# Kernel optimization log

Measured on AMD Instinct MI355X. Metric: run time of the kernel, lower is better.

The kernel has to match this reference:

```python
import jax, jax.numpy as jnp
import numpy as np

N_EMBD = 2048
N_HEAD = 16
N_INNER = 8192
EPS = 1e-5


def _wn_weight(v, g):
    # torch weight_norm with dim=1 on weight [out, in]:
    # w[:, j] = g[j] * v[:, j] / ||v[:, j]||_2
    norm = jnp.sqrt(jnp.sum(v * v, axis=0))  # [in]
    return v * (g / norm)[None, :]


def _layer_norm(x, gamma, beta):
    mu = jnp.mean(x, axis=-1, keepdims=True)
    var = jnp.mean(jnp.square(x - mu), axis=-1, keepdims=True)
    return (x - mu) * jax.lax.rsqrt(var + EPS) * gamma + beta


def setup_inputs() -> dict:
    key = jax.random.key(0)
    ks = jax.random.split(key, 12)
    E, I, H = N_EMBD, N_INNER, N_HEAD
    s = lambda n: 1.0 / np.sqrt(n)
    return {
        "hidden_states": jax.random.normal(ks[0], (2, 2048, E), jnp.float32),
        "ln1_g": jnp.ones((E,), jnp.float32),
        "ln1_b": jnp.zeros((E,), jnp.float32),
        "w_qkv": jax.random.normal(ks[1], (3 * E, E), jnp.float32) * s(E),
        "b_qkv": jnp.zeros((3 * E,), jnp.float32),
        "attn_proj_v": jax.random.normal(ks[2], (E, E), jnp.float32) * s(E),
        "attn_proj_g": jnp.abs(jax.random.normal(ks[3], (E,), jnp.float32)) + 0.5,
        "attn_proj_b": jnp.zeros((E,), jnp.float32),
        "emotion_bias": jax.random.normal(ks[4], (H,), jnp.float32) * 0.1,
        "ln2_g": jnp.ones((E,), jnp.float32),
        "ln2_b": jnp.zeros((E,), jnp.float32),
        "w_fc": jax.random.normal(ks[5], (I, E), jnp.float32) * s(E),
        "b_fc": jnp.zeros((I,), jnp.float32),
        "mlp_proj_v": jax.random.normal(ks[6], (E, I), jnp.float32) * s(I),
        "mlp_proj_g": jnp.abs(jax.random.normal(ks[7], (I,), jnp.float32)) + 0.5,
        "mlp_proj_b": jnp.zeros((E,), jnp.float32),
    }


def reference(hidden_states, ln1_g, ln1_b, w_qkv, b_qkv, attn_proj_v, attn_proj_g,
              attn_proj_b, emotion_bias, ln2_g, ln2_b, w_fc, b_fc,
              mlp_proj_v, mlp_proj_g, mlp_proj_b):
    B, S, E = hidden_states.shape
    H = N_HEAD
    D = E // H

    # --- attention sub-block ---
    residual = hidden_states
    x = _layer_norm(hidden_states, ln1_g, ln1_b)
    qkv = x @ w_qkv.T + b_qkv                       # [B,S,3E]
    q, k, v = jnp.split(qkv, 3, axis=-1)
    q = q.reshape(B, S, H, D).transpose(0, 2, 1, 3)  # [B,H,S,D]
    k = k.reshape(B, S, H, D).transpose(0, 2, 1, 3)
    v = v.reshape(B, S, H, D).transpose(0, 2, 1, 3)

    scores = jnp.einsum("bhqd,bhkd->bhqk", q, k) / jnp.sqrt(jnp.float32(D))
    scores = scores + emotion_bias[None, :, None, None]
    probs = jax.nn.softmax(scores, axis=-1)
    attn = jnp.einsum("bhqk,bhkd->bhqd", probs, v)   # [B,H,S,D]
    attn = attn.transpose(0, 2, 1, 3).reshape(B, S, E)
    w_proj = _wn_weight(attn_proj_v, attn_proj_g)
    attn = attn @ w_proj.T + attn_proj_b

    hidden = attn + residual

    # --- MLP sub-block ---
    residual = hidden
    x = _layer_norm(hidden, ln2_g, ln2_b)
    h = jax.nn.gelu(x @ w_fc.T + b_fc, approximate=False)
    w_proj2 = _wn_weight(mlp_proj_v, mlp_proj_g)
    h = h @ w_proj2.T + mlp_proj_b
    return residual + h
```

## Files before the change

### kernel.cpp

```cpp
#include <hip/hip_runtime.h>
#include <hip/hip_bf16.h>

#define DEVI __device__ __forceinline__

typedef __attribute__((ext_vector_type(8))) __bf16 bf16x8;
typedef __attribute__((ext_vector_type(4))) float f32x4;
typedef __attribute__((ext_vector_type(4))) unsigned short u16x4;
typedef __attribute__((ext_vector_type(8))) unsigned short u16x8;

DEVI unsigned short f2bf(float f) {
  unsigned int u = __float_as_uint(f);
  u += 0x7FFFu + ((u >> 16) & 1u);
  return (unsigned short)(u >> 16);
}
DEVI float bf2f(unsigned short u) {
  return __uint_as_float(((unsigned int)u) << 16);
}

#define GLD16(g, l) __builtin_amdgcn_global_load_lds(                      \
    (const __attribute__((address_space(1))) void*)(g),                    \
    (__attribute__((address_space(3))) void*)(l), 16, 0, 0)


__global__ __launch_bounds__(256) void cast_k(const float* __restrict__ in,
                                              unsigned short* __restrict__ out,
                                              int n4) {
  for (int i = blockIdx.x * 256 + threadIdx.x; i < n4; i += gridDim.x * 256) {
    f32x4 v = ((const f32x4*)in)[i];
    u16x4 o;
    o.x = f2bf(v.x); o.y = f2bf(v.y); o.z = f2bf(v.z); o.w = f2bf(v.w);
    ((u16x4*)out)[i] = o;
  }
}

__global__ __launch_bounds__(256) void colnorm1_k(const float* __restrict__ v,
                                                  float* __restrict__ part,
                                                  int cols) {
  const int tid = threadIdx.x;
  const int g = tid & 127;
  const int s = tid >> 7;
  const int c0 = blockIdx.x * 512;
  const int r0 = blockIdx.y * 64 + s * 32;
  const float* base = v + (size_t)r0 * cols + c0 + g * 4;
  f32x4 acc = {};
#pragma unroll 4
  for (int i = 0; i < 32; ++i) {
    f32x4 x = *(const f32x4*)(base + (size_t)i * cols);
    acc.x += x.x * x.x; acc.y += x.y * x.y;
    acc.z += x.z * x.z; acc.w += x.w * x.w;
  }
  __shared__ f32x4 red[256];
  red[tid] = acc;
  __syncthreads();
  if (s == 0) {
    f32x4 a = red[tid], b = red[tid + 128];
    f32x4 o;
    o.x = a.x + b.x; o.y = a.y + b.y; o.z = a.z + b.z; o.w = a.w + b.w;
    *(f32x4*)(part + (size_t)blockIdx.y * cols + c0 + g * 4) = o;
  }
}

__global__ __launch_bounds__(256) void colnorm2_k(const float* __restrict__ part,
                                                  const float* __restrict__ g,
                                                  float* __restrict__ s,
                                                  int cols, int nrc) {
  const int c = blockIdx.x * 256 + threadIdx.x;
  float acc = 0.f;
  for (int i = 0; i < nrc; ++i) acc += part[(size_t)i * cols + c];
  s[c] = g[c] * rsqrtf(acc);
}

__global__ __launch_bounds__(256) void scale_cast_k(const float* __restrict__ in,
                                                    const float* __restrict__ s,
                                                    unsigned short* __restrict__ out,
                                                    int cols, int n4) {
  const int cmask4 = (cols >> 2) - 1;
  for (int i = blockIdx.x * 256 + threadIdx.x; i < n4; i += gridDim.x * 256) {
    f32x4 v = ((const f32x4*)in)[i];
    f32x4 sv = ((const f32x4*)s)[i & cmask4];
    u16x4 o;
    o.x = f2bf(v.x * sv.x); o.y = f2bf(v.y * sv.y);
    o.z = f2bf(v.z * sv.z); o.w = f2bf(v.w * sv.w);
    ((u16x4*)out)[i] = o;
  }
}

__global__ __launch_bounds__(256) void ln_k(const float* __restrict__ x,
                                            const float* __restrict__ g,
                                            const float* __restrict__ b,
                                            unsigned short* __restrict__ out) {
  const int tid = threadIdx.x, lane = tid & 63, wid = tid >> 6;
  const int row = blockIdx.x;
  const float* xr = x + (size_t)row * 2048;
  f32x4 a0 = ((const f32x4*)xr)[tid];
  f32x4 a1 = ((const f32x4*)xr)[tid + 256];
  float s = a0.x + a0.y + a0.z + a0.w + a1.x + a1.y + a1.z + a1.w;
  float ss = a0.x * a0.x + a0.y * a0.y + a0.z * a0.z + a0.w * a0.w +
             a1.x * a1.x + a1.y * a1.y + a1.z * a1.z + a1.w * a1.w;
#pragma unroll
  for (int m = 1; m < 64; m <<= 1) {
    s += __shfl_xor(s, m);
    ss += __shfl_xor(ss, m);
  }
  __shared__ float red[8];
  if (lane == 0) { red[wid] = s; red[4 + wid] = ss; }
  __syncthreads();
  s = red[0] + red[1] + red[2] + red[3];
  ss = red[4] + red[5] + red[6] + red[7];
  const float mu = s * (1.f / 2048.f);
  const float var = ss * (1.f / 2048.f) - mu * mu;
  const float rs = rsqrtf(var + 1e-5f);
  f32x4 g0 = ((const f32x4*)g)[tid], g1 = ((const f32x4*)g)[tid + 256];
  f32x4 b0 = ((const f32x4*)b)[tid], b1 = ((const f32x4*)b)[tid + 256];
  u16x4 o0, o1;
  o0.x = f2bf((a0.x - mu) * rs * g0.x + b0.x);
  o0.y = f2bf((a0.y - mu) * rs * g0.y + b0.y);
  o0.z = f2bf((a0.z - mu) * rs * g0.z + b0.z);
  o0.w = f2bf((a0.w - mu) * rs * g0.w + b0.w);
  o1.x = f2bf((a1.x - mu) * rs * g1.x + b1.x);
  o1.y = f2bf((a1.y - mu) * rs * g1.y + b1.y);
  o1.z = f2bf((a1.z - mu) * rs * g1.z + b1.z);
  o1.w = f2bf((a1.w - mu) * rs * g1.w + b1.w);
  unsigned short* orow = out + (size_t)row * 2048;
  *(u16x4*)(orow + 4 * tid) = o0;
  *(u16x4*)(orow + 1024 + 4 * tid) = o1;
}

__global__ __launch_bounds__(256) void vtrans_k(const unsigned short* __restrict__ qkv,
                                                unsigned short* __restrict__ vt) {
  __shared__ unsigned short t[64][134];
  const int tid = threadIdx.x;
  const int bh = blockIdx.x >> 5, st = blockIdx.x & 31;
  const int b = bh >> 4, h = bh & 15;
  const unsigned short* vb = qkv + (size_t)(b * 2048 + st * 64) * 6144 + 4096 + h * 128;
#pragma unroll
  for (int i = 0; i < 4; ++i) {
    int f = tid + (i << 8);
    int row = f >> 4, c8 = f & 15;
    u16x8 x = *(const u16x8*)(vb + (size_t)row * 6144 + c8 * 8);
#pragma unroll
    for (int j = 0; j < 4; ++j) {
      unsigned int pk = ((unsigned int)x[2 * j + 1] << 16) | x[2 * j];
      *(unsigned int*)&t[row][c8 * 8 + 2 * j] = pk;
    }
  }
  __syncthreads();
  const int lane = tid & 63, wid = tid >> 6;
  unsigned short* ob = vt + ((size_t)bh << 18) + (st << 6);
#pragma unroll
  for (int j = 0; j < 32; ++j) {
    int d = (wid << 5) + j;
    ob[((size_t)d << 11) + lane] = t[lane][d];
  }
}

__global__ __launch_bounds__(256) void g4red_k(const unsigned short* __restrict__ parts,
                                               const float* __restrict__ bias,
                                               const float* __restrict__ res,
                                               float* __restrict__ out, int n4) {
  const size_t PS = (size_t)4096 * 2048;
  for (int i = blockIdx.x * 256 + threadIdx.x; i < n4; i += gridDim.x * 256) {
    u16x4 a = ((const u16x4*)(parts))[i];
    u16x4 b = ((const u16x4*)(parts + PS))[i];
    u16x4 c = ((const u16x4*)(parts + 2 * PS))[i];
    u16x4 d = ((const u16x4*)(parts + 3 * PS))[i];
    f32x4 r = ((const f32x4*)res)[i];
    f32x4 bb = ((const f32x4*)bias)[i & 511];
    f32x4 o;
    o.x = bf2f(a.x) + bf2f(b.x) + bf2f(c.x) + bf2f(d.x) + r.x + bb.x;
    o.y = bf2f(a.y) + bf2f(b.y) + bf2f(c.y) + bf2f(d.y) + r.y + bb.y;
    o.z = bf2f(a.z) + bf2f(b.z) + bf2f(c.z) + bf2f(d.z) + r.z + bb.z;
    o.w = bf2f(a.w) + bf2f(b.w) + bf2f(c.w) + bf2f(d.w) + r.w + bb.w;
    ((f32x4*)out)[i] = o;
  }
}

struct GemmP {
  const unsigned short* A;
  const unsigned short* B;
  const float* bias;
  const float* res;
  float* outF;
  unsigned short* outH;
  int M, N, K;
};

DEVI void gemm128_body(const GemmP& p, int m0, int n0, int k0, int nk) {
  const int tid = threadIdx.x, lane = tid & 63, wid = tid >> 6;
  const int K = p.K;
  const int wr = wid >> 1, wc = wid & 1;

  __shared__ __align__(16) unsigned short sA[2][4096];
  __shared__ __align__(16) unsigned short sB[2][4096];

  const int c0 = tid, c1 = tid + 256;
  const unsigned short* gA0 = p.A + (size_t)(m0 + (c0 >> 2)) * K + k0 + ((c0 & 3) << 3);
  const unsigned short* gA1 = p.A + (size_t)(m0 + (c1 >> 2)) * K + k0 + ((c1 & 3) << 3);
  const unsigned short* gB0 = p.B + (size_t)(n0 + (c0 >> 2)) * K + k0 + ((c0 & 3) << 3);
  const unsigned short* gB1 = p.B + (size_t)(n0 + (c1 >> 2)) * K + k0 + ((c1 & 3) << 3);
  const int l0 = wid << 9, l1 = (wid << 9) + 2048;

  f32x4 acc[4][4] = {};
  const int arow = (wr << 6) + (lane & 15);
  const int brow = (wc << 6) + (lane & 15);
  const int koff = (lane >> 4) << 3;

#define STAGE128(bufi, t) do { int ko = (t) << 5;       \
    GLD16(gA0 + ko, &sA[bufi][l0]);                     \
    GLD16(gA1 + ko, &sA[bufi][l1]);                     \
    GLD16(gB0 + ko, &sB[bufi][l0]);                     \
    GLD16(gB1 + ko, &sB[bufi][l1]); } while (0)

  STAGE128(0, 0);
  __syncthreads();
  int cur = 0;
  for (int t = 0; t < nk; ++t) {
    if (t + 1 < nk) STAGE128(cur ^ 1, t + 1);
    bf16x8 af[4], bfr[4];
#pragma unroll
    for (int i = 0; i < 4; ++i)
      af[i] = *(const bf16x8*)&sA[cur][(arow + (i << 4)) * 32 + koff];
#pragma unroll
    for (int i = 0; i < 4; ++i)
      bfr[i] = *(const bf16x8*)&sB[cur][(brow + (i << 4)) * 32 + koff];
#pragma unroll
    for (int i = 0; i < 4; ++i)
#pragma unroll
      for (int j = 0; j < 4; ++j)
        acc[i][j] = __builtin_amdgcn_mfma_f32_16x16x32_bf16(af[i], bfr[j], acc[i][j], 0, 0, 0);
    __syncthreads();
    cur ^= 1;
  }
#undef STAGE128

  const int rbase = m0 + (wr << 6) + ((lane >> 4) << 2);
  const int cbase = n0 + (wc << 6) + (lane & 15);
#pragma unroll
  for (int mi = 0; mi < 4; ++mi) {
#pragma unroll
    for (int ni = 0; ni < 4; ++ni) {
      const int col = cbase + (ni << 4);
#pragma unroll
      for (int r = 0; r < 4; ++r) {
        const int row = rbase + (mi << 4) + r;
        const size_t o = (size_t)row * p.N + col;
        p.outF[o] = acc[mi][ni][r] + p.bias[col] + p.res[o];
      }
    }
  }
}

__global__ __launch_bounds__(256) void g2_proj128(GemmP p) {
  const int x = blockIdx.x & 7, i = blockIdx.x >> 3;
  const int bm = (x >> 1) * 8 + (i >> 3);
  const int bn = (x & 1) * 8 + (i & 7);
  gemm128_body(p, bm << 7, bn << 7, 0, p.K >> 5);
}

DEVI void setup256(const GemmP& p, int m0, int n0, int k0,
                   const unsigned short*& gsA0, const unsigned short*& gsA1,
                   const unsigned short*& gsB0, const unsigned short*& gsB1) {
  const int tid = threadIdx.x;
  int r_[2], c_[2];
#pragma unroll
  for (int j = 0; j < 2; ++j) {
    int d = tid * 16 + j * 8192;
    int w = (d & 1023) ^ (((d >> 9) & 1) << 5);
    r_[j] = ((d >> 10) << 4) + (w >> 6);
    c_[j] = (w & 63) >> 1;
  }
  gsA0 = p.A + (size_t)(m0 + r_[0]) * p.K + k0 + c_[0];
  gsA1 = p.A + (size_t)(m0 + r_[1]) * p.K + k0 + c_[1];
  gsB0 = p.B + (size_t)(n0 + r_[0]) * p.K + k0 + c_[0];
  gsB1 = p.B + (size_t)(n0 + r_[1]) * p.K + k0 + c_[1];
}

template <int EPI>
DEVI void epi256(const GemmP& p, f32x4 (&acc)[8][4], int m0, int n0,
                 unsigned short* outH) {
  const int lane = threadIdx.x & 63, wid = threadIdx.x >> 6;
  const int wr = wid >> 2, wc = wid & 3;
  const int lr = lane & 15, lk = lane >> 4;
  const int rbase = m0 + wr * 128 + (lk << 2);
  const int cbase = n0 + wc * 64 + lr;
#pragma unroll
  for (int m = 0; m < 8; ++m) {
#pragma unroll
    for (int n = 0; n < 4; ++n) {
      const int col = cbase + (n << 4);
      const float bb = (EPI == 5) ? 0.f : p.bias[col];
#pragma unroll
      for (int r = 0; r < 4; ++r) {
        const int row = rbase + (m << 4) + r;
        float v = acc[m][n][r] + bb;
        if constexpr (EPI == 2) {
          float y = 0.7978845608028654f * (v + 0.044715f * v * v * v);
          float u = __expf(2.f * y);
          v = (y > 40.f) ? v : v * (u / (u + 1.f));
        }
        outH[(size_t)row * p.N + col] = f2bf(v);
      }
    }
  }
}

DEVI void gemm8p_body(const GemmP& p, unsigned short* lds_raw, int m0, int n0) {
  const int tid = threadIdx.x, lane = tid & 63, wid = tid >> 6;
  const int wr = wid >> 2, wc = wid & 3;
  const int lr = lane & 15, lk = lane >> 4;
  const int fb = (lr * 64 + lk * 16) ^ ((lr & 8) << 2);

  const unsigned short *gsA0, *gsA1, *gsB0, *gsB1;
  setup256(p, m0, n0, 0, gsA0, gsA1, gsB0, gsB1);

#define STAGE_A8(b, kt) do { unsigned short* _d = lds_raw + ((b) << 14);       \
    GLD16(gsA0 + ((size_t)(kt) << 5), _d + (tid << 3));                        \
    GLD16(gsA1 + ((size_t)(kt) << 5), _d + 4096 + (tid << 3)); } while (0)
#define STAGE_B8(b, kt) do { unsigned short* _d = lds_raw + ((b) << 14) + 8192;\
    GLD16(gsB0 + ((size_t)(kt) << 5), _d + (tid << 3));                        \
    GLD16(gsB1 + ((size_t)(kt) << 5), _d + 4096 + (tid << 3)); } while (0)

  f32x4 acc[8][4] = {};
  const int NK = p.K >> 5;

  STAGE_A8(0, 0); STAGE_B8(0, 0);
  STAGE_A8(1, 1); STAGE_B8(1, 1);
  STAGE_A8(2, 2); STAGE_B8(2, 2);
  asm volatile("s_waitcnt vmcnt(8)" ::: "memory");
  __builtin_amdgcn_s_barrier();

  for (int t = 0; t < NK; ++t) {
    const int bi = t & 3;
    const char* tA = (const char*)(lds_raw + (bi << 14));
    const char* tB = (const char*)(lds_raw + (bi << 14) + 8192);
    bf16x8 a_[4], b_[4];
#pragma unroll
    for (int n = 0; n < 4; ++n)
      b_[n] = *(const bf16x8*)(tB + (((wc << 2) + n) << 10) + fb);
#pragma unroll
    for (int m = 0; m < 4; ++m)
      a_[m] = *(const bf16x8*)(tA + (((wr << 3) + m) << 10) + fb);
    if (t + 3 < NK) STAGE_A8((t + 3) & 3, t + 3);
    __builtin_amdgcn_s_barrier();
    asm volatile("s_waitcnt lgkmcnt(0)" ::: "memory");
    __builtin_amdgcn_sched_barrier(0);
    __builtin_amdgcn_s_setprio(1);
#pragma unroll
    for (int m = 0; m < 4; ++m)
#pragma unroll
      for (int n = 0; n < 4; ++n)
        acc[m][n] = __builtin_amdgcn_mfma_f32_16x16x32_bf16(a_[m], b_[n], acc[m][n], 0, 0, 0);
    __builtin_amdgcn_s_setprio(0);
    __builtin_amdgcn_s_barrier();
#pragma unroll
    for (int m = 0; m < 4; ++m)
      a_[m] = *(const bf16x8*)(tA + (((wr << 3) + 4 + m) << 10) + fb);
    if (t + 3 < NK) STAGE_B8((t + 3) & 3, t + 3);
    if (t + 3 < NK)      asm volatile("s_waitcnt vmcnt(8)" ::: "memory");
    else if (t + 2 < NK) asm volatile("s_waitcnt vmcnt(4)" ::: "memory");
    else if (t + 1 < NK) asm volatile("s_waitcnt vmcnt(0)" ::: "memory");
    __builtin_amdgcn_s_barrier();
    asm volatile("s_waitcnt lgkmcnt(0)" ::: "memory");
    __builtin_amdgcn_sched_barrier(0);
    __builtin_amdgcn_s_setprio(1);
#pragma unroll
    for (int m = 0; m < 4; ++m)
#pragma unroll
      for (int n = 0; n < 4; ++n)
        acc[4 + m][n] = __builtin_amdgcn_mfma_f32_16x16x32_bf16(a_[m], b_[n], acc[4 + m][n], 0, 0, 0);
    __builtin_amdgcn_s_setprio(0);
    __builtin_amdgcn_s_barrier();
  }
#undef STAGE_A8
#undef STAGE_B8
  epi256<2>(p, acc, m0, n0, p.outH);
}

template <int EPI>
DEVI void gemm2p_body(const GemmP& p, unsigned short* lds_raw, int m0, int n0,
                      int k0, int nk, unsigned short* outH) {
  const int tid = threadIdx.x, lane = tid & 63, wid = tid >> 6;
  const int wr = wid >> 2, wc = wid & 3;
  const int lr = lane & 15, lk = lane >> 4;
  const int fb = (lr * 64 + lk * 16) ^ ((lr & 8) << 2);

  const unsigned short *gsA0, *gsA1, *gsB0, *gsB1;
  setup256(p, m0, n0, k0, gsA0, gsA1, gsB0, gsB1);

#define STG2(b, kt) do { unsigned short* _d = lds_raw + ((b) << 14);     \
    GLD16(gsA0 + ((size_t)(kt) << 5), _d + (tid << 3));                  \
    GLD16(gsA1 + ((size_t)(kt) << 5), _d + 4096 + (tid << 3));           \
    GLD16(gsB0 + ((size_t)(kt) << 5), _d + 8192 + (tid << 3));           \
    GLD16(gsB1 + ((size_t)(kt) << 5), _d + 12288 + (tid << 3)); } while (0)

  f32x4 acc[8][4] = {};
  STG2(0, 0);
  __syncthreads();
  int cur = 0;
  for (int t = 0; t < nk; ++t) {
    if (t + 1 < nk) STG2(cur ^ 1, t + 1);
    const char* tA = (const char*)(lds_raw + (cur << 14));
    const char* tB = tA + 16384;
    bf16x8 a_[8], b_[4];
#pragma unroll
    for (int n = 0; n < 4; ++n)
      b_[n] = *(const bf16x8*)(tB + (((wc << 2) + n) << 10) + fb);
#pragma unroll
    for (int m = 0; m < 8; ++m)
      a_[m] = *(const bf16x8*)(tA + (((wr << 3) + m) << 10) + fb);
#pragma unroll
    for (int m = 0; m < 8; ++m)
#pragma unroll
      for (int n = 0; n < 4; ++n)
        acc[m][n] = __builtin_amdgcn_mfma_f32_16x16x32_bf16(a_[m], b_[n], acc[m][n], 0, 0, 0);
    __syncthreads();
    cur ^= 1;
  }
#undef STG2
  epi256<EPI>(p, acc, m0, n0, outH);
}

__global__ __launch_bounds__(512, 2) void g1_qkv256(GemmP p) {
  extern __shared__ unsigned short lds_raw[];
  const int x = blockIdx.x & 7, i = blockIdx.x >> 3;
  const int bm = (x & 1) * 8 + (i & 7);
  const int bn = (x >> 1) * 6 + (i >> 3);
  gemm2p_body<0>(p, lds_raw, bm << 8, bn << 8, 0, p.K >> 5, p.outH);
}
__global__ __launch_bounds__(512, 2) void g3a_fc8p(GemmP p) {
  extern __shared__ unsigned short lds_raw[];
  const int x = blockIdx.x & 7, i = blockIdx.x >> 3;
  const int bm = (x >> 2) * 4 + (i >> 3);
  const int bn = (x & 3) * 8 + (i & 7);
  gemm8p_body(p, lds_raw, bm << 8, bn << 8);
}
__global__ __launch_bounds__(512, 2) void g3b_fc2p(GemmP p) {
  extern __shared__ unsigned short lds_raw[];
  const int x = blockIdx.x & 7, i = blockIdx.x >> 3;
  const int bm = (x >> 2) * 4 + (i >> 3);
  const int bn = (x & 3) * 8 + (i & 7);
  gemm2p_body<2>(p, lds_raw, 2048 + (bm << 8), bn << 8, 0, p.K >> 5, p.outH);
}
__global__ __launch_bounds__(512, 2) void g4_splitk256(GemmP p) {
  extern __shared__ unsigned short lds_raw[];
  const int x = blockIdx.x & 7, i = blockIdx.x >> 3;
  const int ks = x & 3;
  const int bm = (x >> 2) * 8 + (i >> 3);
  const int bn = i & 7;
  unsigned short* outH = p.outH + (size_t)ks * 4096 * 2048;
  gemm2p_body<5>(p, lds_raw, bm << 8, bn << 8, ks << 11, 64, outH);
}

__global__ __launch_bounds__(512) void attn_k(const unsigned short* __restrict__ qkv,
                                              const unsigned short* __restrict__ Vt,
                                              unsigned short* __restrict__ O) {
  const int tid = threadIdx.x, lane = tid & 63, wid = tid >> 6;
  const int bid = blockIdx.x;
  const int pos = bid >> 3;
  const int bh = (bid & 7) * 4 + (pos >> 4);
  const int qt = pos & 15;
  const int q0 = qt * 128 + wid * 16;
  const int b = bh >> 4, h = bh & 15;

  __shared__ __align__(16) unsigned short sK[64 * 128];
  __shared__ __align__(16) unsigned short sV[128 * 64];
  __shared__ __align__(16) unsigned short sP[8][16 * 68];

  const unsigned short* Qb = qkv + (size_t)(b * 2048) * 6144 + h * 128;
  const unsigned short* Kb = qkv + (size_t)(b * 2048) * 6144 + 2048 + h * 128;
  const unsigned short* Vb = Vt + ((size_t)bh << 18);

  bf16x8 qf[4];
  {
    const unsigned short* qp = Qb + (size_t)(q0 + (lane & 15)) * 6144 + ((lane >> 4) << 3);
#pragma unroll
    for (int kk = 0; kk < 4; ++kk) qf[kk] = *(const bf16x8*)(qp + kk * 32);
  }

  int koffs[2], voffs[2];
#pragma unroll
  for (int i = 0; i < 2; ++i) {
    const int c = tid + (i << 9);
    const int kv = c >> 4, jj = c & 15;
    const int js = (jj & 8) | ((jj ^ kv) & 7);
    koffs[i] = kv * 6144 + (js << 3);
    const int d = c >> 3, j2 = c & 7;
    const int js2 = j2 ^ (d & 7);
    voffs[i] = d * 2048 + (js2 << 3);
  }
  u16x8 kreg[2], vreg[2];
  auto PREF = [&](int kt) {
    const int kv0 = kt << 6;
    const unsigned short* kb = Kb + (size_t)kv0 * 6144;
#pragma unroll
    for (int i = 0; i < 2; ++i) {
      kreg[i] = *(const u16x8*)(kb + koffs[i]);
      vreg[i] = *(const u16x8*)(Vb + kv0 + voffs[i]);
    }
  };

  f32x4 oacc[8] = {};
  float mrun = -3e38f, lrun = 0.f;
  PREF(0);

  for (int kt = 0; kt < 32; ++kt) {
#pragma unroll
    for (int i = 0; i < 2; ++i) {
      const int c8 = (tid + (i << 9)) << 3;
      *(u16x8*)&sK[c8] = kreg[i];
      *(u16x8*)&sV[c8] = vreg[i];
    }
    __syncthreads();
    if (kt + 1 < 32) PREF(kt + 1);

    f32x4 sc[4] = {};
    __builtin_amdgcn_s_setprio(1);
#pragma unroll
    for (int ti = 0; ti < 4; ++ti) {
#pragma unroll
      for (int kk = 0; kk < 4; ++kk) {
        const int row = (ti << 4) + (lane & 15);
        int bo = (row << 8) + (kk << 6) + ((lane >> 4) << 4);
        bo ^= (row & 7) << 4;
        bf16x8 kf = *(const bf16x8*)((const char*)sK + bo);
        sc[ti] = __builtin_amdgcn_mfma_f32_16x16x32_bf16(kf, qf[kk], sc[ti], 0, 0, 0);
      }
    }
    __builtin_amdgcn_s_setprio(0);

    float pv[16];
    float mx = -3e38f;
#pragma unroll
    for (int ti = 0; ti < 4; ++ti)
#pragma unroll
      for (int r = 0; r < 4; ++r) {
        float x = sc[ti][r] * 0.08838834764831845f;
        pv[(ti << 2) + r] = x;
        mx = fmaxf(mx, x);
      }
    mx = fmaxf(mx, __shfl_xor(mx, 16));
    mx = fmaxf(mx, __shfl_xor(mx, 32));

    float corr = 1.f;
    if (!__all(mx - mrun <= 8.f)) {
      const float mnew = fmaxf(mrun, mx);
      corr = __expf(mrun - mnew);
      mrun = mnew;
      float fr[4];
#pragma unroll
      for (int r = 0; r < 4; ++r) fr[r] = __shfl(corr, ((lane >> 4) << 2) + r);
#pragma unroll
      for (int di = 0; di < 8; ++di)
#pragma unroll
        for (int r = 0; r < 4; ++r) oacc[di][r] *= fr[r];
    }
    float psum = 0.f;
#pragma unroll
    for (int i2 = 0; i2 < 16; ++i2) {
      float e = __expf(pv[i2] - mrun);
      pv[i2] = e;
      psum += e;
    }
    psum += __shfl_xor(psum, 16);
    psum += __shfl_xor(psum, 32);
    lrun = lrun * corr + psum;

    unsigned short* prow = &sP[wid][(lane & 15) * 68];
#pragma unroll
    for (int ti = 0; ti < 4; ++ti) {
      u16x4 w4;
      w4.x = f2bf(pv[(ti << 2) + 0]);
      w4.y = f2bf(pv[(ti << 2) + 1]);
      w4.z = f2bf(pv[(ti << 2) + 2]);
      w4.w = f2bf(pv[(ti << 2) + 3]);
      *(u16x4*)&prow[(ti << 4) + ((lane >> 4) << 2)] = w4;
    }

    __builtin_amdgcn_s_setprio(1);
#pragma unroll
    for (int di = 0; di < 8; ++di) {
#pragma unroll
      for (int ks = 0; ks < 2; ++ks) {
        bf16x8 pf = *(const bf16x8*)((const char*)&sP[wid][0] +
                                     (lane & 15) * 136 + (ks << 6) + ((lane >> 4) << 4));
        const int dr = (di << 4) + (lane & 15);
        int bo = (dr << 7) + (ks << 6) + ((lane >> 4) << 4);
        bo ^= (dr & 7) << 4;
        bf16x8 vf = *(const bf16x8*)((const char*)sV + bo);
        oacc[di] = __builtin_amdgcn_mfma_f32_16x16x32_bf16(pf, vf, oacc[di], 0, 0, 0);
      }
    }
    __builtin_amdgcn_s_setprio(0);
    __syncthreads();
  }

  float il[4];
#pragma unroll
  for (int r = 0; r < 4; ++r) il[r] = 1.f / __shfl(lrun, ((lane >> 4) << 2) + r);
  const size_t obase = ((size_t)(b * 2048 + q0)) * 2048 + h * 128;
#pragma unroll
  for (int di = 0; di < 8; ++di)
#pragma unroll
    for (int r = 0; r < 4; ++r) {
      const size_t o = obase + (size_t)(((lane >> 4) << 2) + r) * 2048 + (di << 4) + (lane & 15);
      O[o] = f2bf(oacc[di][r] * il[r]);
    }
}


extern "C" void kernel_launch(void* const* d_in, const int* in_sizes, int n_in,
                              void* d_out, int out_size, void* d_ws, size_t ws_size,
                              hipStream_t stream) {
  (void)in_sizes; (void)n_in; (void)out_size; (void)ws_size;
  const float* hidden = (const float*)d_in[0];
  const float* ln1_g = (const float*)d_in[1];
  const float* ln1_b = (const float*)d_in[2];
  const float* w_qkv = (const float*)d_in[3];
  const float* b_qkv = (const float*)d_in[4];
  const float* apv = (const float*)d_in[5];
  const float* apg = (const float*)d_in[6];
  const float* apb = (const float*)d_in[7];
  const float* ln2_g = (const float*)d_in[9];
  const float* ln2_b = (const float*)d_in[10];
  const float* w_fc = (const float*)d_in[11];
  const float* b_fc = (const float*)d_in[12];
  const float* mpv = (const float*)d_in[13];
  const float* mpg = (const float*)d_in[14];
  const float* mpb = (const float*)d_in[15];

  char* w = (char*)d_ws;
  const size_t MBs = 1ull << 20;
  unsigned short* xln = (unsigned short*)(w + 0);
  float* hidden2 = (float*)(w + 0);
  unsigned short* vtbuf = (unsigned short*)(w + 32 * MBs);
  unsigned short* hbuf = (unsigned short*)(w + 32 * MBs);
  unsigned short* qkv = (unsigned short*)(w + 96 * MBs);
  unsigned short* wfc_bf = (unsigned short*)(w + 96 * MBs);
  unsigned short* partH = (unsigned short*)(w + 96 * MBs);
  unsigned short* xln2 = (unsigned short*)(w + 128 * MBs);
  unsigned short* attn_out = (unsigned short*)(w + 144 * MBs);
  unsigned short* wqkv_bf = (unsigned short*)(w + 160 * MBs);
  unsigned short* w2_bf = (unsigned short*)(w + 160 * MBs);
  unsigned short* wproj_bf = (unsigned short*)(w + 192 * MBs);
  float* s_attn = (float*)(w + 200 * MBs);
  float* s_mlp = (float*)(w + 200 * MBs + 32768);
  float* part_attn = (float*)(w + 201 * MBs);
  float* part_mlp = (float*)(w + 202 * MBs);

  hipFuncSetAttribute((const void*)g1_qkv256, hipFuncAttributeMaxDynamicSharedMemorySize, 65536);
  hipFuncSetAttribute((const void*)g3a_fc8p, hipFuncAttributeMaxDynamicSharedMemorySize, 131072);
  hipFuncSetAttribute((const void*)g3b_fc2p, hipFuncAttributeMaxDynamicSharedMemorySize, 65536);
  hipFuncSetAttribute((const void*)g4_splitk256, hipFuncAttributeMaxDynamicSharedMemorySize, 65536);

  cast_k<<<2048, 256, 0, stream>>>(w_qkv, wqkv_bf, (6144 * 2048) / 4);
  colnorm1_k<<<dim3(4, 32), 256, 0, stream>>>(apv, part_attn, 2048);
  colnorm2_k<<<8, 256, 0, stream>>>(part_attn, apg, s_attn, 2048, 32);
  scale_cast_k<<<2048, 256, 0, stream>>>(apv, s_attn, wproj_bf, 2048, (2048 * 2048) / 4);
  colnorm1_k<<<dim3(16, 32), 256, 0, stream>>>(mpv, part_mlp, 8192);
  colnorm2_k<<<32, 256, 0, stream>>>(part_mlp, mpg, s_mlp, 8192, 32);

  ln_k<<<4096, 256, 0, stream>>>(hidden, ln1_g, ln1_b, xln);

  GemmP p1 = {xln, wqkv_bf, b_qkv, nullptr, nullptr, qkv, 4096, 6144, 2048};
  g1_qkv256<<<384, 512, 65536, stream>>>(p1);

  vtrans_k<<<1024, 256, 0, stream>>>(qkv, vtbuf);

  attn_k<<<512, 512, 0, stream>>>(qkv, vtbuf, attn_out);

  cast_k<<<2048, 256, 0, stream>>>(w_fc, wfc_bf, (8192 * 2048) / 4);
  scale_cast_k<<<4096, 256, 0, stream>>>(mpv, s_mlp, w2_bf, 8192, (2048 * 8192) / 4);

  GemmP p2 = {attn_out, wproj_bf, apb, hidden, hidden2, nullptr, 4096, 2048, 2048};
  g2_proj128<<<512, 256, 0, stream>>>(p2);

  ln_k<<<4096, 256, 0, stream>>>(hidden2, ln2_g, ln2_b, xln2);

  GemmP p3 = {xln2, wfc_bf, b_fc, nullptr, nullptr, hbuf, 4096, 8192, 2048};
  g3a_fc8p<<<256, 512, 131072, stream>>>(p3);
  g3b_fc2p<<<256, 512, 65536, stream>>>(p3);

  GemmP p4 = {hbuf, w2_bf, mpb, nullptr, nullptr, partH, 4096, 2048, 8192};
  g4_splitk256<<<512, 512, 65536, stream>>>(p4);
  g4red_k<<<2048, 256, 0, stream>>>(partH, mpb, hidden2, (float*)d_out,
                                    (4096 * 2048) / 4);
}
```

Measured before the change: 862.5 us.

## Merge split FC GEMM into one double-buffered launch and pad attention P tile

The FC GEMM was split into two launches: a 4-stage pipelined kernel using 128KB of LDS for the first half of the rows and a double-buffered kernel for the second half. Both are replaced by a single 512-block launch of the double-buffered 256x256 body with a new tile swizzle. This removes one launch and lets all blocks share one schedule, at the cost of the deeper prefetch pipeline. Separately, the attention kernel's per-warp P buffer row stride is padded from 68 to 72 elements, which changes LDS bank mapping and 16-byte alignment of the vector reads.

```diff
diff --git a/kernel.cpp b/kernel.cpp
--- a/kernel.cpp
+++ b/kernel.cpp
@@ -304,78 +304,6 @@
   }
 }
 
-DEVI void gemm8p_body(const GemmP& p, unsigned short* lds_raw, int m0, int n0) {
-  const int tid = threadIdx.x, lane = tid & 63, wid = tid >> 6;
-  const int wr = wid >> 2, wc = wid & 3;
-  const int lr = lane & 15, lk = lane >> 4;
-  const int fb = (lr * 64 + lk * 16) ^ ((lr & 8) << 2);
-
-  const unsigned short *gsA0, *gsA1, *gsB0, *gsB1;
-  setup256(p, m0, n0, 0, gsA0, gsA1, gsB0, gsB1);
-
-#define STAGE_A8(b, kt) do { unsigned short* _d = lds_raw + ((b) << 14);       \
-    GLD16(gsA0 + ((size_t)(kt) << 5), _d + (tid << 3));                        \
-    GLD16(gsA1 + ((size_t)(kt) << 5), _d + 4096 + (tid << 3)); } while (0)
-#define STAGE_B8(b, kt) do { unsigned short* _d = lds_raw + ((b) << 14) + 8192;\
-    GLD16(gsB0 + ((size_t)(kt) << 5), _d + (tid << 3));                        \
-    GLD16(gsB1 + ((size_t)(kt) << 5), _d + 4096 + (tid << 3)); } while (0)
-
-  f32x4 acc[8][4] = {};
-  const int NK = p.K >> 5;
-
-  STAGE_A8(0, 0); STAGE_B8(0, 0);
-  STAGE_A8(1, 1); STAGE_B8(1, 1);
-  STAGE_A8(2, 2); STAGE_B8(2, 2);
-  asm volatile("s_waitcnt vmcnt(8)" ::: "memory");
-  __builtin_amdgcn_s_barrier();
-
-  for (int t = 0; t < NK; ++t) {
-    const int bi = t & 3;
-    const char* tA = (const char*)(lds_raw + (bi << 14));
-    const char* tB = (const char*)(lds_raw + (bi << 14) + 8192);
-    bf16x8 a_[4], b_[4];
-#pragma unroll
-    for (int n = 0; n < 4; ++n)
-      b_[n] = *(const bf16x8*)(tB + (((wc << 2) + n) << 10) + fb);
-#pragma unroll
-    for (int m = 0; m < 4; ++m)
-      a_[m] = *(const bf16x8*)(tA + (((wr << 3) + m) << 10) + fb);
-    if (t + 3 < NK) STAGE_A8((t + 3) & 3, t + 3);
-    __builtin_amdgcn_s_barrier();
-    asm volatile("s_waitcnt lgkmcnt(0)" ::: "memory");
-    __builtin_amdgcn_sched_barrier(0);
-    __builtin_amdgcn_s_setprio(1);
-#pragma unroll
-    for (int m = 0; m < 4; ++m)
-#pragma unroll
-      for (int n = 0; n < 4; ++n)
-        acc[m][n] = __builtin_amdgcn_mfma_f32_16x16x32_bf16(a_[m], b_[n], acc[m][n], 0, 0, 0);
-    __builtin_amdgcn_s_setprio(0);
-    __builtin_amdgcn_s_barrier();
-#pragma unroll
-    for (int m = 0; m < 4; ++m)
-      a_[m] = *(const bf16x8*)(tA + (((wr << 3) + 4 + m) << 10) + fb);
-    if (t + 3 < NK) STAGE_B8((t + 3) & 3, t + 3);
-    if (t + 3 < NK)      asm volatile("s_waitcnt vmcnt(8)" ::: "memory");
-    else if (t + 2 < NK) asm volatile("s_waitcnt vmcnt(4)" ::: "memory");
-    else if (t + 1 < NK) asm volatile("s_waitcnt vmcnt(0)" ::: "memory");
-    __builtin_amdgcn_s_barrier();
-    asm volatile("s_waitcnt lgkmcnt(0)" ::: "memory");
-    __builtin_amdgcn_sched_barrier(0);
-    __builtin_amdgcn_s_setprio(1);
-#pragma unroll
-    for (int m = 0; m < 4; ++m)
-#pragma unroll
-      for (int n = 0; n < 4; ++n)
-        acc[4 + m][n] = __builtin_amdgcn_mfma_f32_16x16x32_bf16(a_[m], b_[n], acc[4 + m][n], 0, 0, 0);
-    __builtin_amdgcn_s_setprio(0);
-    __builtin_amdgcn_s_barrier();
-  }
-#undef STAGE_A8
-#undef STAGE_B8
-  epi256<2>(p, acc, m0, n0, p.outH);
-}
-
 template <int EPI>
 DEVI void gemm2p_body(const GemmP& p, unsigned short* lds_raw, int m0, int n0,
                       int k0, int nk, unsigned short* outH) {
@@ -427,19 +355,12 @@
   const int bn = (x >> 1) * 6 + (i >> 3);
   gemm2p_body<0>(p, lds_raw, bm << 8, bn << 8, 0, p.K >> 5, p.outH);
 }
-__global__ __launch_bounds__(512, 2) void g3a_fc8p(GemmP p) {
+__global__ __launch_bounds__(512, 2) void g3_fc256(GemmP p) {
   extern __shared__ unsigned short lds_raw[];
   const int x = blockIdx.x & 7, i = blockIdx.x >> 3;
-  const int bm = (x >> 2) * 4 + (i >> 3);
-  const int bn = (x & 3) * 8 + (i & 7);
-  gemm8p_body(p, lds_raw, bm << 8, bn << 8);
-}
-__global__ __launch_bounds__(512, 2) void g3b_fc2p(GemmP p) {
-  extern __shared__ unsigned short lds_raw[];
-  const int x = blockIdx.x & 7, i = blockIdx.x >> 3;
-  const int bm = (x >> 2) * 4 + (i >> 3);
-  const int bn = (x & 3) * 8 + (i & 7);
-  gemm2p_body<2>(p, lds_raw, 2048 + (bm << 8), bn << 8, 0, p.K >> 5, p.outH);
+  const int bm = (x & 1) * 8 + (i & 7);
+  const int bn = (x >> 1) * 8 + (i >> 3);
+  gemm2p_body<2>(p, lds_raw, bm << 8, bn << 8, 0, p.K >> 5, p.outH);
 }
 __global__ __launch_bounds__(512, 2) void g4_splitk256(GemmP p) {
   extern __shared__ unsigned short lds_raw[];
@@ -464,7 +385,7 @@
 
   __shared__ __align__(16) unsigned short sK[64 * 128];
   __shared__ __align__(16) unsigned short sV[128 * 64];
-  __shared__ __align__(16) unsigned short sP[8][16 * 68];
+  __shared__ __align__(16) unsigned short sP[8][16 * 72];
 
   const unsigned short* Qb = qkv + (size_t)(b * 2048) * 6144 + h * 128;
   const unsigned short* Kb = qkv + (size_t)(b * 2048) * 6144 + 2048 + h * 128;
@@ -565,7 +486,7 @@
     psum += __shfl_xor(psum, 32);
     lrun = lrun * corr + psum;
 
-    unsigned short* prow = &sP[wid][(lane & 15) * 68];
+    unsigned short* prow = &sP[wid][(lane & 15) * 72];
 #pragma unroll
     for (int ti = 0; ti < 4; ++ti) {
       u16x4 w4;
@@ -582,7 +503,7 @@
 #pragma unroll
       for (int ks = 0; ks < 2; ++ks) {
         bf16x8 pf = *(const bf16x8*)((const char*)&sP[wid][0] +
-                                     (lane & 15) * 136 + (ks << 6) + ((lane >> 4) << 4));
+                                     (lane & 15) * 144 + (ks << 6) + ((lane >> 4) << 4));
         const int dr = (di << 4) + (lane & 15);
         int bo = (dr << 7) + (ks << 6) + ((lane >> 4) << 4);
         bo ^= (dr & 7) << 4;
@@ -648,8 +569,7 @@
   float* part_mlp = (float*)(w + 202 * MBs);
 
   hipFuncSetAttribute((const void*)g1_qkv256, hipFuncAttributeMaxDynamicSharedMemorySize, 65536);
-  hipFuncSetAttribute((const void*)g3a_fc8p, hipFuncAttributeMaxDynamicSharedMemorySize, 131072);
-  hipFuncSetAttribute((const void*)g3b_fc2p, hipFuncAttributeMaxDynamicSharedMemorySize, 65536);
+  hipFuncSetAttribute((const void*)g3_fc256, hipFuncAttributeMaxDynamicSharedMemorySize, 65536);
   hipFuncSetAttribute((const void*)g4_splitk256, hipFuncAttributeMaxDynamicSharedMemorySize, 65536);
 
   cast_k<<<2048, 256, 0, stream>>>(w_qkv, wqkv_bf, (6144 * 2048) / 4);
@@ -677,8 +597,7 @@
   ln_k<<<4096, 256, 0, stream>>>(hidden2, ln2_g, ln2_b, xln2);
 
   GemmP p3 = {xln2, wfc_bf, b_fc, nullptr, nullptr, hbuf, 4096, 8192, 2048};
-  g3a_fc8p<<<256, 512, 131072, stream>>>(p3);
-  g3b_fc2p<<<256, 512, 65536, stream>>>(p3);
+  g3_fc256<<<512, 512, 65536, stream>>>(p3);
 
   GemmP p4 = {hbuf, w2_bf, mpb, nullptr, nullptr, partH, 4096, 2048, 8192};
   g4_splitk256<<<512, 512, 65536, stream>>>(p4);
```

After: 746.2 us. -13.5%, faster.
